# Kernel optimization log

Hardware: AMD Instinct MI355X
Metric: run time of the kernel (lower is better)

The kernel has to match this reference:

```python
import jax, jax.numpy as jnp
import numpy as np

DIM = 768
HEADS = 12
DIM_HEAD = 64
INNER = HEADS * DIM_HEAD  # 768
SCALE = DIM_HEAD ** -0.5


def setup_inputs() -> dict:
    key = jax.random.key(0)
    k1, k2, k3, k4 = jax.random.split(key, 4)
    b, n = 8, 1024
    x = jax.random.normal(k1, (b, n, DIM), dtype=jnp.float32)
    # fused QKV projection, no bias: y = x @ w_qkv  -> [b, n, 3*inner]
    w_qkv = jax.random.normal(k2, (DIM, 3 * INNER), dtype=jnp.float32) * (DIM ** -0.5)
    # output projection with bias
    w_out = jax.random.normal(k3, (INNER, DIM), dtype=jnp.float32) * (INNER ** -0.5)
    b_out = jax.random.normal(k4, (DIM,), dtype=jnp.float32) * 0.02
    return {"x": x, "w_qkv": w_qkv, "w_out": w_out, "b_out": b_out}


def reference(x, w_qkv, w_out, b_out):
    b, n, _ = x.shape
    qkv = jnp.einsum('bnd,de->bne', x, w_qkv)  # [b, n, 3*inner]
    q, k, v = jnp.split(qkv, 3, axis=-1)
    # 'b n (h d) -> b h n d'
    def split_heads(t):
        return t.reshape(b, n, HEADS, DIM_HEAD).transpose(0, 2, 1, 3)
    q, k, v = split_heads(q), split_heads(k), split_heads(v)
    dots = jnp.einsum('bhid,bhjd->bhij', q, k) * SCALE  # [b, h, n, n]
    attn = jax.nn.softmax(dots, axis=-1)
    out = jnp.einsum('bhij,bhjd->bhid', attn, v)  # [b, h, n, d]
    out = out.transpose(0, 2, 1, 3).reshape(b, n, INNER)  # 'b h n d -> b n (h d)'
    return jnp.einsum('bne,ed->bnd', out, w_out) + b_out
```

## Files before the change

kernel.cpp:

```cpp
#include <hip/hip_runtime.h>

typedef unsigned short u16;
typedef __bf16 bf16x8 __attribute__((ext_vector_type(8)));
typedef float f32x4 __attribute__((ext_vector_type(4)));

__device__ inline u16 f2bf(float f) {
    union { float f; unsigned int u; } a; a.f = f;
    unsigned int u = a.u + 0x7fffu + ((a.u >> 16) & 1u);
    return (u16)(u >> 16);
}

__device__ __forceinline__ void cp16(const void* g, void* l) {
    __builtin_amdgcn_global_load_lds(
        (const __attribute__((address_space(1))) unsigned int*)g,
        (__attribute__((address_space(3))) unsigned int*)l, 16, 0, 0);
}

__global__ __launch_bounds__(256) void prep(
    const float* __restrict__ x, const float* __restrict__ wq,
    const float* __restrict__ wo, u16* __restrict__ xbf,
    u16* __restrict__ wtq, u16* __restrict__ wto)
{
    int bid = blockIdx.x;
    if (bid < 3072) {
        size_t base = ((size_t)bid * 256 + threadIdx.x) * 8;
        float4 f0 = *(const float4*)&x[base];
        float4 f1 = *(const float4*)&x[base + 4];
        union { u16 s[8]; uint4 v; } t;
        t.s[0]=f2bf(f0.x); t.s[1]=f2bf(f0.y); t.s[2]=f2bf(f0.z); t.s[3]=f2bf(f0.w);
        t.s[4]=f2bf(f1.x); t.s[5]=f2bf(f1.y); t.s[6]=f2bf(f1.z); t.s[7]=f2bf(f1.w);
        *(uint4*)&xbf[base] = t.v;
        return;
    }
    __shared__ u16 tile[32][33];
    const float* in; u16* outp; int N, bx, by;
    if (bid < 3072 + 1728) { int t = bid - 3072; in = wq; outp = wtq; N = 2304; bx = t % 72; by = t / 72; }
    else                   { int t = bid - 4800; in = wo; outp = wto; N = 768;  bx = t % 24; by = t / 24; }
    int n0 = bx * 32, k0 = by * 32;
    int tx = threadIdx.x & 31, ty = threadIdx.x >> 5;
    #pragma unroll
    for (int r = ty; r < 32; r += 8)
        tile[r][tx] = f2bf(in[(size_t)(k0 + r) * N + n0 + tx]);
    __syncthreads();
    #pragma unroll
    for (int r = ty; r < 32; r += 8)
        outp[(size_t)(n0 + r) * 768 + k0 + tx] = tile[tx][r];
}

__global__ __launch_bounds__(256) void gemm_qkv(
    const u16* __restrict__ A, const u16* __restrict__ Bt,
    u16* __restrict__ q_out, u16* __restrict__ k_out, u16* __restrict__ v_out)
{
    const int K = 768;
    __shared__ __align__(16) u16 As[128 * 32];
    __shared__ __align__(16) u16 Bs[128 * 32];

    int tid = threadIdx.x;
    int lane = tid & 63, wave = tid >> 6;
    int quad = lane >> 4, l16 = lane & 15;
    int wm = wave >> 1, wn = wave & 1;
    int m0 = blockIdx.y * 128, n0 = blockIdx.x * 128;

    f32x4 acc[4][4];
    #pragma unroll
    for (int i = 0; i < 4; i++)
        #pragma unroll
        for (int j = 0; j < 4; j++) acc[i][j] = (f32x4){0.f, 0.f, 0.f, 0.f};

    int r0 = tid >> 2, c0 = (tid & 3) * 8;
    for (int kt = 0; kt < K; kt += 32) {
        cp16(&A [(size_t)(m0 + r0)      * K + kt + c0], &As[(size_t)tid * 8]);
        cp16(&A [(size_t)(m0 + 64 + r0) * K + kt + c0], &As[(size_t)(256 + tid) * 8]);
        cp16(&Bt[(size_t)(n0 + r0)      * K + kt + c0], &Bs[(size_t)tid * 8]);
        cp16(&Bt[(size_t)(n0 + 64 + r0) * K + kt + c0], &Bs[(size_t)(256 + tid) * 8]);
        __syncthreads();
        bf16x8 af[4], bfr[4];
        #pragma unroll
        for (int i = 0; i < 4; i++) af[i]  = *(const bf16x8*)&As[(wm * 64 + i * 16 + l16) * 32 + quad * 8];
        #pragma unroll
        for (int j = 0; j < 4; j++) bfr[j] = *(const bf16x8*)&Bs[(wn * 64 + j * 16 + l16) * 32 + quad * 8];
        #pragma unroll
        for (int i = 0; i < 4; i++)
            #pragma unroll
            for (int j = 0; j < 4; j++)
                acc[i][j] = __builtin_amdgcn_mfma_f32_16x16x32_bf16(af[i], bfr[j], acc[i][j], 0, 0, 0);
        __syncthreads();
    }

    #pragma unroll
    for (int i = 0; i < 4; i++) {
        int mbase = m0 + wm * 64 + i * 16 + quad * 4;
        int b = mbase >> 10, npos = mbase & 1023;
        #pragma unroll
        for (int j = 0; j < 4; j++) {
            int n = n0 + wn * 64 + j * 16 + l16;
            int part  = n >= 1536 ? 2 : (n >= 768 ? 1 : 0);
            int inner = n - part * 768;
            int h = inner >> 6, dd = inner & 63;
            if (part == 2) {
                union { u16 s[4]; uint2 v; } pk;
                #pragma unroll
                for (int r = 0; r < 4; r++) pk.s[r] = f2bf(acc[i][j][r]);
                *(uint2*)&v_out[((size_t)((b * 12 + h) * 64 + dd)) * 1024 + npos] = pk.v;
            } else {
                #pragma unroll
                for (int r = 0; r < 4; r++) {
                    size_t idx = ((size_t)((b * 12 + h) * 1024 + npos + r)) * 64 + dd;
                    float v = acc[i][j][r];
                    if (part == 0) q_out[idx] = f2bf(v * 0.18033688011112042f);
                    else           k_out[idx] = f2bf(v);
                }
            }
        }
    }
}

__global__ __launch_bounds__(256) void attn128(
    u16* __restrict__ QO, const u16* __restrict__ Kg, const u16* __restrict__ Vtg)
{
    __shared__ __align__(16) u16 Ks[64 * 64];
    __shared__ __align__(16) u16 Vs[64 * 64];

    int tid = threadIdx.x;
    int lane = tid & 63, wave = tid >> 6;
    int quad = lane >> 4, l16 = lane & 15;
    int bh = blockIdx.y;
    int q0 = blockIdx.x * 128;
    const size_t head_base = (size_t)bh * 65536;

    size_t qoff[2];
    bf16x8 qf[2][2];
    #pragma unroll
    for (int qs = 0; qs < 2; qs++) {
        qoff[qs] = head_base + (size_t)(q0 + wave * 32 + qs * 16 + l16) * 64;
        qf[qs][0] = *(const bf16x8*)&QO[qoff[qs] + quad * 8];
        qf[qs][1] = *(const bf16x8*)&QO[qoff[qs] + 32 + quad * 8];
    }

    f32x4 Oacc[4][2];
    #pragma unroll
    for (int dt = 0; dt < 4; dt++)
        #pragma unroll
        for (int qs = 0; qs < 2; qs++) Oacc[dt][qs] = (f32x4){0.f, 0.f, 0.f, 0.f};
    float l_part[2] = {0.f, 0.f};

    int srow = tid >> 3, sg = tid & 7;
    for (int j0 = 0; j0 < 1024; j0 += 64) {
        #pragma unroll
        for (int it = 0; it < 2; ++it) {
            int e = it * 256 + tid, row = it * 32 + srow, gs = sg ^ (row & 7);
            cp16(&Kg [head_base + (size_t)(j0 + row) * 64 + gs * 8], &Ks[(size_t)e * 8]);
            cp16(&Vtg[head_base + (size_t)row * 1024 + j0 + gs * 8], &Vs[(size_t)e * 8]);
        }
        __syncthreads();

        f32x4 s4[4][2];
        #pragma unroll
        for (int nt = 0; nt < 4; nt++) {
            int R = nt * 16 + l16;
            bf16x8 kf0 = *(const bf16x8*)&Ks[R * 64 + ((quad       ^ (R & 7)) * 8)];
            bf16x8 kf1 = *(const bf16x8*)&Ks[R * 64 + (((quad + 4) ^ (R & 7)) * 8)];
            #pragma unroll
            for (int qs = 0; qs < 2; qs++) {
                f32x4 s = (f32x4){0.f, 0.f, 0.f, 0.f};
                s = __builtin_amdgcn_mfma_f32_16x16x32_bf16(kf0, qf[qs][0], s, 0, 0, 0);
                s = __builtin_amdgcn_mfma_f32_16x16x32_bf16(kf1, qf[qs][1], s, 0, 0, 0);
                s4[nt][qs] = s;
            }
        }

        #pragma unroll
        for (int nt = 0; nt < 4; nt++)
            #pragma unroll
            for (int qs = 0; qs < 2; qs++)
                #pragma unroll
                for (int r = 0; r < 4; r++) {
                    float p = __builtin_amdgcn_exp2f(s4[nt][qs][r]);
                    s4[nt][qs][r] = p;
                    l_part[qs] += p;
                }

        #pragma unroll
        for (int h = 0; h < 2; h++) {
            union { u16 s[8]; bf16x8 v; } pk[2];
            #pragma unroll
            for (int qs = 0; qs < 2; qs++)
                #pragma unroll
                for (int r = 0; r < 4; r++) {
                    pk[qs].s[r]     = f2bf(s4[2 * h][qs][r]);
                    pk[qs].s[4 + r] = f2bf(s4[2 * h + 1][qs][r]);
                }
            int lg0 = 4 * h + (quad >> 1), lg1 = lg0 + 2;
            int off = (quad & 1) * 4;
            #pragma unroll
            for (int dt = 0; dt < 4; dt++) {
                int drow = dt * 16 + l16;
                union { u16 s[8]; bf16x8 v; } vk;
                *(uint2*)&vk.s[0] = *(const uint2*)&Vs[drow * 64 + (lg0 ^ (drow & 7)) * 8 + off];
                *(uint2*)&vk.s[4] = *(const uint2*)&Vs[drow * 64 + (lg1 ^ (drow & 7)) * 8 + off];
                #pragma unroll
                for (int qs = 0; qs < 2; qs++)
                    Oacc[dt][qs] = __builtin_amdgcn_mfma_f32_16x16x32_bf16(vk.v, pk[qs].v, Oacc[dt][qs], 0, 0, 0);
            }
        }
        __syncthreads();
    }

    #pragma unroll
    for (int qs = 0; qs < 2; qs++) {
        float l = l_part[qs];
        l += __shfl_xor(l, 16);
        l += __shfl_xor(l, 32);
        float rl = __builtin_amdgcn_rcpf(l);
        #pragma unroll
        for (int dt = 0; dt < 4; dt++) {
            union { u16 s[4]; uint2 v; } ok;
            #pragma unroll
            for (int r = 0; r < 4; r++) ok.s[r] = f2bf(Oacc[dt][qs][r] * rl);
            *(uint2*)&QO[qoff[qs] + dt * 16 + quad * 4] = ok.v;
        }
    }
}

__global__ __launch_bounds__(256) void gemm_out(
    const u16* __restrict__ Qg, const u16* __restrict__ Bt,
    const float* __restrict__ bias, float* __restrict__ out)
{
    const int K = 768;
    __shared__ __align__(16) u16 As[128 * 32];
    __shared__ __align__(16) u16 Bs[128 * 32];

    int tid = threadIdx.x;
    int lane = tid & 63, wave = tid >> 6;
    int quad = lane >> 4, l16 = lane & 15;
    int wm = wave >> 1, wn = wave & 1;
    int m0 = blockIdx.y * 128, n0 = blockIdx.x * 128;

    f32x4 acc[4][4];
    #pragma unroll
    for (int i = 0; i < 4; i++)
        #pragma unroll
        for (int j = 0; j < 4; j++) acc[i][j] = (f32x4){0.f, 0.f, 0.f, 0.f};

    int r0 = tid >> 2, c0 = (tid & 3) * 8;
    for (int kt = 0; kt < K; kt += 32) {
        int k = kt + c0, h = k >> 6, dd = k & 63;
        #pragma unroll
        for (int it = 0; it < 2; ++it) {
            int m = m0 + it * 64 + r0, b = m >> 10, npos = m & 1023;
            cp16(&Qg[(((size_t)(b * 12 + h) * 1024 + npos) << 6) + dd],
                 &As[(size_t)(it * 256 + tid) * 8]);
            cp16(&Bt[(size_t)(n0 + it * 64 + r0) * K + kt + c0],
                 &Bs[(size_t)(it * 256 + tid) * 8]);
        }
        __syncthreads();
        bf16x8 af[4], bfr[4];
        #pragma unroll
        for (int i = 0; i < 4; i++) af[i]  = *(const bf16x8*)&As[(wm * 64 + i * 16 + l16) * 32 + quad * 8];
        #pragma unroll
        for (int j = 0; j < 4; j++) bfr[j] = *(const bf16x8*)&Bs[(wn * 64 + j * 16 + l16) * 32 + quad * 8];
        #pragma unroll
        for (int i = 0; i < 4; i++)
            #pragma unroll
            for (int j = 0; j < 4; j++)
                acc[i][j] = __builtin_amdgcn_mfma_f32_16x16x32_bf16(af[i], bfr[j], acc[i][j], 0, 0, 0);
        __syncthreads();
    }

    #pragma unroll
    for (int i = 0; i < 4; i++) {
        int mbase = m0 + wm * 64 + i * 16 + quad * 4;
        #pragma unroll
        for (int j = 0; j < 4; j++) {
            int n = n0 + wn * 64 + j * 16 + l16;
            float bv = bias[n];
            #pragma unroll
            for (int r = 0; r < 4; r++)
                out[(size_t)(mbase + r) * 768 + n] = acc[i][j][r] + bv;
        }
    }
}

extern "C" void kernel_launch(void* const* d_in, const int* in_sizes, int n_in,
                              void* d_out, int out_size, void* d_ws, size_t ws_size,
                              hipStream_t stream) {
    const float* x     = (const float*)d_in[0];
    const float* w_qkv = (const float*)d_in[1];
    const float* w_out = (const float*)d_in[2];
    const float* b_out = (const float*)d_in[3];
    float* out = (float*)d_out;

    char* ws = (char*)d_ws;
    u16* wtq  = (u16*)(ws);
    u16* wto  = (u16*)(ws + 3538944);
    u16* Qbuf = (u16*)(ws + 4718592);
    u16* xbf  = (u16*)(ws + 17301504);
    u16* Kbuf = (u16*)d_out;
    u16* Vbuf = (u16*)d_out + 6291456;

    prep<<<dim3(5376), 256, 0, stream>>>(x, w_qkv, w_out, xbf, wtq, wto);
    gemm_qkv<<<dim3(18, 64), 256, 0, stream>>>(xbf, wtq, Qbuf, Kbuf, Vbuf);
    attn128<<<dim3(8, 96), 256, 0, stream>>>(Qbuf, Kbuf, Vbuf);
    gemm_out<<<dim3(6, 64), 256, 0, stream>>>(Qbuf, wto, b_out, out);
}
```

Before: 210.9 us.

## Double GEMM K-tile to 64 with XOR-swizzled LDS and staged QKV epilogue

Both projection GEMMs now stage 64-wide K tiles instead of 32, which halves the number of barrier pairs per output tile. The LDS layout is XOR-swizzled on 16-byte groups so the fragment reads avoid bank conflicts. The QKV epilogue first writes results through shared memory, then emits coalesced 16-byte global stores for Q, K and the transposed V, replacing scattered 2-byte and 8-byte stores. This doubles LDS use per block, which may reduce occupancy, and adds an extra barrier in the epilogue.

```diff
diff --git a/kernel.cpp b/kernel.cpp
--- a/kernel.cpp
+++ b/kernel.cpp
@@ -52,8 +52,8 @@
     u16* __restrict__ q_out, u16* __restrict__ k_out, u16* __restrict__ v_out)
 {
     const int K = 768;
-    __shared__ __align__(16) u16 As[128 * 32];
-    __shared__ __align__(16) u16 Bs[128 * 32];
+    __shared__ __align__(16) u16 As[128 * 64];
+    __shared__ __align__(16) u16 Bs[128 * 64];
 
     int tid = threadIdx.x;
     int lane = tid & 63, wave = tid >> 6;
@@ -67,50 +67,88 @@
         #pragma unroll
         for (int j = 0; j < 4; j++) acc[i][j] = (f32x4){0.f, 0.f, 0.f, 0.f};
 
-    int r0 = tid >> 2, c0 = (tid & 3) * 8;
-    for (int kt = 0; kt < K; kt += 32) {
-        cp16(&A [(size_t)(m0 + r0)      * K + kt + c0], &As[(size_t)tid * 8]);
-        cp16(&A [(size_t)(m0 + 64 + r0) * K + kt + c0], &As[(size_t)(256 + tid) * 8]);
-        cp16(&Bt[(size_t)(n0 + r0)      * K + kt + c0], &Bs[(size_t)tid * 8]);
-        cp16(&Bt[(size_t)(n0 + 64 + r0) * K + kt + c0], &Bs[(size_t)(256 + tid) * 8]);
-        __syncthreads();
-        bf16x8 af[4], bfr[4];
-        #pragma unroll
-        for (int i = 0; i < 4; i++) af[i]  = *(const bf16x8*)&As[(wm * 64 + i * 16 + l16) * 32 + quad * 8];
-        #pragma unroll
-        for (int j = 0; j < 4; j++) bfr[j] = *(const bf16x8*)&Bs[(wn * 64 + j * 16 + l16) * 32 + quad * 8];
+    int r0 = tid >> 3, cg = tid & 7;
+    for (int kt = 0; kt < K; kt += 64) {
+        #pragma unroll
+        for (int it = 0; it < 4; ++it) {
+            int row = it * 32 + r0;
+            int g = cg ^ (row & 7);
+            cp16(&A [(size_t)(m0 + row) * K + kt + g * 8], &As[(size_t)(it * 256 + tid) * 8]);
+            cp16(&Bt[(size_t)(n0 + row) * K + kt + g * 8], &Bs[(size_t)(it * 256 + tid) * 8]);
+        }
+        __syncthreads();
+        #pragma unroll
+        for (int ko = 0; ko < 2; ko++) {
+            bf16x8 af[4], bfr[4];
+            #pragma unroll
+            for (int i = 0; i < 4; i++) {
+                int R = wm * 64 + i * 16 + l16;
+                af[i] = *(const bf16x8*)&As[R * 64 + (((ko * 4 + quad) ^ (R & 7)) * 8)];
+            }
+            #pragma unroll
+            for (int j = 0; j < 4; j++) {
+                int R = wn * 64 + j * 16 + l16;
+                bfr[j] = *(const bf16x8*)&Bs[R * 64 + (((ko * 4 + quad) ^ (R & 7)) * 8)];
+            }
+            #pragma unroll
+            for (int i = 0; i < 4; i++)
+                #pragma unroll
+                for (int j = 0; j < 4; j++)
+                    acc[i][j] = __builtin_amdgcn_mfma_f32_16x16x32_bf16(af[i], bfr[j], acc[i][j], 0, 0, 0);
+        }
+        __syncthreads();
+    }
+
+    int M0 = m0 + wm * 64, N0 = n0 + wn * 64;
+    int part = N0 >= 1536 ? 2 : (N0 >= 768 ? 1 : 0);
+    int h = (N0 - part * 768) >> 6;
+    int b = M0 >> 10, npos0 = M0 & 1023;
+    u16* ep = (wave < 2 ? As : Bs) + (wave & 1) * 4096;
+
+    if (part != 2) {
+        float scale = (part == 0) ? 0.18033688011112042f : 1.0f;
+        u16* gbase = (part == 0 ? q_out : k_out) + (((size_t)(b * 12 + h) * 1024 + npos0) << 6);
         #pragma unroll
         for (int i = 0; i < 4; i++)
             #pragma unroll
-            for (int j = 0; j < 4; j++)
-                acc[i][j] = __builtin_amdgcn_mfma_f32_16x16x32_bf16(af[i], bfr[j], acc[i][j], 0, 0, 0);
-        __syncthreads();
-    }
-
-    #pragma unroll
-    for (int i = 0; i < 4; i++) {
-        int mbase = m0 + wm * 64 + i * 16 + quad * 4;
-        int b = mbase >> 10, npos = mbase & 1023;
-        #pragma unroll
-        for (int j = 0; j < 4; j++) {
-            int n = n0 + wn * 64 + j * 16 + l16;
-            int part  = n >= 1536 ? 2 : (n >= 768 ? 1 : 0);
-            int inner = n - part * 768;
-            int h = inner >> 6, dd = inner & 63;
-            if (part == 2) {
+            for (int j = 0; j < 4; j++) {
+                int dd = j * 16 + l16;
+                #pragma unroll
+                for (int r = 0; r < 4; r++) {
+                    int np = i * 16 + quad * 4 + r;
+                    ep[np * 64 + (((dd >> 3) ^ (np & 7)) * 8) + (dd & 7)] =
+                        f2bf(acc[i][j][r] * scale);
+                }
+            }
+        __syncthreads();
+        #pragma unroll
+        for (int t = 0; t < 8; t++) {
+            int idx = t * 512 + lane * 8;
+            int np = idx >> 6;
+            int slot = ((lane & 7) ^ (np & 7));
+            uint4 v = *(const uint4*)&ep[np * 64 + slot * 8];
+            *(uint4*)&gbase[idx] = v;
+        }
+    } else {
+        #pragma unroll
+        for (int i = 0; i < 4; i++)
+            #pragma unroll
+            for (int j = 0; j < 4; j++) {
+                int dd = j * 16 + l16;
+                int npg = i * 2 + (quad >> 1);
+                int sub = (quad & 1) * 4;
                 union { u16 s[4]; uint2 v; } pk;
                 #pragma unroll
                 for (int r = 0; r < 4; r++) pk.s[r] = f2bf(acc[i][j][r]);
-                *(uint2*)&v_out[((size_t)((b * 12 + h) * 64 + dd)) * 1024 + npos] = pk.v;
-            } else {
-                #pragma unroll
-                for (int r = 0; r < 4; r++) {
-                    size_t idx = ((size_t)((b * 12 + h) * 1024 + npos + r)) * 64 + dd;
-                    float v = acc[i][j][r];
-                    if (part == 0) q_out[idx] = f2bf(v * 0.18033688011112042f);
-                    else           k_out[idx] = f2bf(v);
-                }
-            }
+                *(uint2*)&ep[dd * 64 + ((npg ^ (dd & 7)) * 8) + sub] = pk.v;
+            }
+        __syncthreads();
+        #pragma unroll
+        for (int t = 0; t < 8; t++) {
+            int dd = t * 8 + (lane >> 3);
+            int npg = lane & 7;
+            uint4 v = *(const uint4*)&ep[dd * 64 + ((npg ^ (dd & 7)) * 8)];
+            *(uint4*)&v_out[((size_t)((b * 12 + h) * 64 + dd)) * 1024 + npos0 + npg * 8] = v;
         }
     }
 }
@@ -227,8 +265,8 @@
     const float* __restrict__ bias, float* __restrict__ out)
 {
     const int K = 768;
-    __shared__ __align__(16) u16 As[128 * 32];
-    __shared__ __align__(16) u16 Bs[128 * 32];
+    __shared__ __align__(16) u16 As[128 * 64];
+    __shared__ __align__(16) u16 Bs[128 * 64];
 
     int tid = threadIdx.x;
     int lane = tid & 63, wave = tid >> 6;
@@ -242,28 +280,39 @@
         #pragma unroll
         for (int j = 0; j < 4; j++) acc[i][j] = (f32x4){0.f, 0.f, 0.f, 0.f};
 
-    int r0 = tid >> 2, c0 = (tid & 3) * 8;
-    for (int kt = 0; kt < K; kt += 32) {
-        int k = kt + c0, h = k >> 6, dd = k & 63;
-        #pragma unroll
-        for (int it = 0; it < 2; ++it) {
-            int m = m0 + it * 64 + r0, b = m >> 10, npos = m & 1023;
-            cp16(&Qg[(((size_t)(b * 12 + h) * 1024 + npos) << 6) + dd],
+    int r0 = tid >> 3, cg = tid & 7;
+    for (int kt = 0; kt < K; kt += 64) {
+        int h = kt >> 6;
+        #pragma unroll
+        for (int it = 0; it < 4; ++it) {
+            int row = it * 32 + r0;
+            int g = cg ^ (row & 7);
+            int m = m0 + row, b = m >> 10, npos = m & 1023;
+            cp16(&Qg[(((size_t)(b * 12 + h) * 1024 + npos) << 6) + g * 8],
                  &As[(size_t)(it * 256 + tid) * 8]);
-            cp16(&Bt[(size_t)(n0 + it * 64 + r0) * K + kt + c0],
+            cp16(&Bt[(size_t)(n0 + row) * K + kt + g * 8],
                  &Bs[(size_t)(it * 256 + tid) * 8]);
         }
         __syncthreads();
-        bf16x8 af[4], bfr[4];
-        #pragma unroll
-        for (int i = 0; i < 4; i++) af[i]  = *(const bf16x8*)&As[(wm * 64 + i * 16 + l16) * 32 + quad * 8];
-        #pragma unroll
-        for (int j = 0; j < 4; j++) bfr[j] = *(const bf16x8*)&Bs[(wn * 64 + j * 16 + l16) * 32 + quad * 8];
-        #pragma unroll
-        for (int i = 0; i < 4; i++)
-            #pragma unroll
-            for (int j = 0; j < 4; j++)
-                acc[i][j] = __builtin_amdgcn_mfma_f32_16x16x32_bf16(af[i], bfr[j], acc[i][j], 0, 0, 0);
+        #pragma unroll
+        for (int ko = 0; ko < 2; ko++) {
+            bf16x8 af[4], bfr[4];
+            #pragma unroll
+            for (int i = 0; i < 4; i++) {
+                int R = wm * 64 + i * 16 + l16;
+                af[i] = *(const bf16x8*)&As[R * 64 + (((ko * 4 + quad) ^ (R & 7)) * 8)];
+            }
+            #pragma unroll
+            for (int j = 0; j < 4; j++) {
+                int R = wn * 64 + j * 16 + l16;
+                bfr[j] = *(const bf16x8*)&Bs[R * 64 + (((ko * 4 + quad) ^ (R & 7)) * 8)];
+            }
+            #pragma unroll
+            for (int i = 0; i < 4; i++)
+                #pragma unroll
+                for (int j = 0; j < 4; j++)
+                    acc[i][j] = __builtin_amdgcn_mfma_f32_16x16x32_bf16(af[i], bfr[j], acc[i][j], 0, 0, 0);
+        }
         __syncthreads();
     }
 
```

Result: faster. 201.2 us (-4.6%).
